# Optimization experiments

Measured on AMD Instinct MI355X. Metric: run time of the kernel, lower is better.

## Reference

```python
import jax, jax.numpy as jnp
import numpy as np

WIN = (2, 7, 7)  # (H, W, D) window size

def _relative_position_index(H, W, D):
    coords = np.stack(np.meshgrid(np.arange(H), np.arange(W), np.arange(D), indexing='ij'))
    cf = coords.reshape(3, -1)  # [3, N]
    rel = cf[:, :, None] - cf[:, None, :]  # [3, N, N]
    rel = rel.transpose(1, 2, 0).copy()
    rel[:, :, 0] += H - 1
    rel[:, :, 1] += W - 1
    rel[:, :, 2] += D - 1
    rel[:, :, 0] *= (2 * W - 1) * (2 * D - 1)
    rel[:, :, 1] *= 2 * D - 1
    return jnp.asarray(rel.sum(-1), dtype=jnp.int32)  # [N, N]

def setup_inputs() -> dict:
    key = jax.random.key(0)
    ks = jax.random.split(key, 7)
    H, W, D = WIN
    N = H * W * D          # 98
    C = 192
    nh = 6
    num_windows = 64
    B_ = 8 * num_windows   # 512
    x = jax.random.normal(ks[0], (B_, N, C), dtype=jnp.float32)
    # shifted-window attention mask: 0 for allowed pairs, -100 for masked
    mask = jnp.where(jax.random.uniform(ks[1], (num_windows, N, N)) < 0.9, 0.0, -100.0).astype(jnp.float32)
    qkv_w = jax.random.normal(ks[2], (3 * C, C), dtype=jnp.float32) * 0.02
    qkv_b = jnp.zeros((3 * C,), dtype=jnp.float32)
    out_w = jax.random.normal(ks[3], (C, C), dtype=jnp.float32) * 0.02
    out_b = jnp.zeros((C,), dtype=jnp.float32)
    table_len = (2 * H - 1) * (2 * W - 1) * (2 * D - 1)  # 507
    bias_table = jax.random.normal(ks[4], (table_len, nh), dtype=jnp.float32) * 0.02
    rel_index = _relative_position_index(H, W, D)
    return {"x": x, "mask": mask, "qkv_w": qkv_w, "qkv_b": qkv_b,
            "out_w": out_w, "out_b": out_b, "bias_table": bias_table,
            "rel_index": rel_index}

def reference(x, mask, qkv_w, qkv_b, out_w, out_b, bias_table, rel_index):
    B_, N, C = x.shape
    nh = bias_table.shape[1]
    d = C // nh
    scale = d ** (-0.5)
    qkv = (x @ qkv_w.T + qkv_b).reshape(B_, N, 3, nh, d)
    qkv = qkv.transpose(2, 0, 3, 1, 4)          # [3, B_, nh, N, d]
    q, k, v = qkv[0], qkv[1], qkv[2]
    attn = jnp.einsum('bhnd,bhmd->bhnm', q, k) * scale   # [B_, nh, N, N]
    bias = bias_table[rel_index]                 # [N, N, nh]
    attn = attn + bias.transpose(2, 0, 1)[None]  # add relative position bias
    nw = mask.shape[0]
    attn = attn.reshape(B_ // nw, nw, nh, N, N) + mask[None, :, None]
    attn = attn.reshape(B_, nh, N, N)
    p = jax.nn.softmax(attn, axis=-1)
    out = jnp.einsum('bhnm,bhmd->bhnd', p, v)    # [B_, nh, N, d]
    out = out.transpose(0, 2, 1, 3).reshape(B_, N, C)
    return out @ out_w.T + out_b
```

## Files before the change

kernel.cpp:

```cpp
#include <hip/hip_runtime.h>

typedef __attribute__((ext_vector_type(8))) __bf16 bf16x8;
typedef __attribute__((ext_vector_type(4))) float f32x4;
typedef __attribute__((ext_vector_type(8))) unsigned short us8;
typedef __attribute__((ext_vector_type(4))) unsigned short us4;

#define NTOK 98
#define CDIM 192
#define NH 6
#define NWIN 64
#define BWIN 512
#define MROWS (BWIN * NTOK)
#define NN (NTOK * NTOK)
#define SCALE 0.17677669529663687f

#define PREP_BM (NWIN * NH * NN)
#define PREP_WQ (3 * CDIM * CDIM)
#define PREP_TOT (PREP_BM + PREP_WQ)

__device__ __forceinline__ unsigned short f2b(float f) {
  unsigned u = __builtin_bit_cast(unsigned, f);
  u += 0x7FFFu + ((u >> 16) & 1u);
  return (unsigned short)(u >> 16);
}

__device__ __forceinline__ bf16x8 ldfrag(const unsigned short* p) {
  return __builtin_bit_cast(bf16x8, *(const us8*)p);
}

__global__ __launch_bounds__(256) void k_prep(
    const float* __restrict__ table, const int* __restrict__ relidx,
    const float* __restrict__ mask, const float* __restrict__ wq,
    float* __restrict__ bm, unsigned short* __restrict__ wqb) {
  int idx = blockIdx.x * 256 + threadIdx.x;
  if (idx < PREP_BM) {
    int w = idx / (NH * NN);
    int r = idx - w * NH * NN;
    int h = r / NN, ij = r - h * NN;
    bm[idx] = table[relidx[ij] * NH + h] + mask[w * NN + ij];
    return;
  }
  int i2 = idx - PREP_BM;
  if (i2 < PREP_WQ) wqb[i2] = f2b(wq[i2]);
}

__global__ __launch_bounds__(256) void k_qkv(
    const float* __restrict__ x, const unsigned short* __restrict__ wqb,
    const float* __restrict__ bias, unsigned short* __restrict__ qkv) {
  __shared__ unsigned short As[128 * 200];
  __shared__ unsigned short Bs[64 * 200];
  const int tid = threadIdx.x;
  const int m0 = blockIdx.x * 128;
  for (int it = 0; it < 24; ++it) {
    int q = it * 256 + tid;
    int row = q / 48, c4 = q - row * 48;
    float4 v = *(const float4*)(x + (m0 + row) * CDIM + c4 * 4);
    us4 u = {f2b(v.x), f2b(v.y), f2b(v.z), f2b(v.w)};
    *(us4*)&As[row * 200 + c4 * 4] = u;
  }
  const int lane = tid & 63;
  const int l15 = lane & 15, hi = lane >> 4;
  const int wr = (tid >> 6) >> 1, wc = (tid >> 6) & 1;
  __syncthreads();
  for (int j = 0; j < 9; ++j) {
    for (int it = 0; it < 6; ++it) {
      int q = it * 256 + tid;
      int row = q / 24, c8 = q - row * 24;
      *(us8*)&Bs[row * 200 + c8 * 8] = *(const us8*)(wqb + (j * 64 + row) * CDIM + c8 * 8);
    }
    __syncthreads();
    f32x4 acc[4][2];
#pragma unroll
    for (int fr = 0; fr < 4; ++fr) { acc[fr][0] = (f32x4)0.f; acc[fr][1] = (f32x4)0.f; }
#pragma unroll
    for (int ks = 0; ks < 6; ++ks) {
      int k0 = ks * 32 + hi * 8;
      bf16x8 b0 = ldfrag(&Bs[(wc * 32 + l15) * 200 + k0]);
      bf16x8 b1 = ldfrag(&Bs[(wc * 32 + 16 + l15) * 200 + k0]);
#pragma unroll
      for (int fr = 0; fr < 4; ++fr) {
        bf16x8 a = ldfrag(&As[(wr * 64 + fr * 16 + l15) * 200 + k0]);
        acc[fr][0] = __builtin_amdgcn_mfma_f32_16x16x32_bf16(a, b0, acc[fr][0], 0, 0, 0);
        acc[fr][1] = __builtin_amdgcn_mfma_f32_16x16x32_bf16(a, b1, acc[fr][1], 0, 0, 0);
      }
    }
    __syncthreads();
#pragma unroll
    for (int fr = 0; fr < 4; ++fr)
#pragma unroll
      for (int fc = 0; fc < 2; ++fc) {
        int colb = j * 64 + wc * 32 + fc * 16;
        int t = (colb >= 2 * CDIM) ? 2 : (colb >= CDIM ? 1 : 0);
        int head = (colb >> 5) - t * NH;
        int d = (colb & 31) + l15;
        long pbase = ((long)(t * NH + head) * MROWS) * 32 + d;
#pragma unroll
        for (int r = 0; r < 4; ++r) {
          int row = m0 + wr * 64 + fr * 16 + hi * 4 + r;
          float v = acc[fr][fc][r] + bias[colb + l15];
          if (t == 0) v *= SCALE;
          qkv[pbase + (long)row * 32] = f2b(v);
        }
      }
  }
}

__global__ __launch_bounds__(448, 6) void k_attn(
    const unsigned short* __restrict__ qkv, const float* __restrict__ bm,
    unsigned short* __restrict__ ao) {
  __shared__ unsigned short Vt[32 * 136];
  __shared__ unsigned short P[112 * 136];
  const int tid = threadIdx.x;
  const int h = blockIdx.x % NH;
  const int b = blockIdx.x / NH;
  const int wnd = b & (NWIN - 1);
  const int lane = tid & 63, wv = tid >> 6;
  const int l15 = lane & 15, hi = lane >> 4;
  const long rb = (long)b * NTOK;
  const unsigned short* qp = qkv + ((long)h * MROWS + rb) * 32;
  const unsigned short* kp = qkv + ((long)(NH + h) * MROWS + rb) * 32;
  const unsigned short* vp = qkv + ((long)(2 * NH + h) * MROWS + rb) * 32;
  {
    int row = tid >> 2, q = tid & 3;
    if (row < NTOK) {
      us8 vv = *(const us8*)(vp + row * 32 + q * 8);
#pragma unroll
      for (int i = 0; i < 8; ++i) Vt[(q * 8 + i) * 136 + row] = vv[i];
    }
    for (int i = tid; i < 32 * 38; i += 448) {
      int dd = i / 38, n = NTOK + (i - dd * 38);
      Vt[dd * 136 + n] = 0;
    }
    for (int i = tid; i < 112 * 16; i += 448)
      P[(i >> 4) * 136 + 112 + (i & 15)] = 0;
  }
  int qn = wv * 16 + l15;
  us8 qu = (us8)0;
  if (qn < NTOK) qu = *(const us8*)(qp + qn * 32 + hi * 8);
  bf16x8 qf = __builtin_bit_cast(bf16x8, qu);
  __syncthreads();
  f32x4 sacc[7];
#pragma unroll
  for (int tc = 0; tc < 7; ++tc) {
    int rowc = tc * 16 + l15;
    rowc = rowc > 97 ? 97 : rowc;
    bf16x8 kb = ldfrag(kp + rowc * 32 + hi * 8);
    sacc[tc] = __builtin_amdgcn_mfma_f32_16x16x32_bf16(qf, kb, (f32x4)0.f, 0, 0, 0);
  }
  const float* bmp = bm + (size_t)(wnd * NH + h) * NN;
  float rsum[4];
#pragma unroll
  for (int r = 0; r < 4; ++r) {
    int row = wv * 16 + hi * 4 + r;
    int rowc = row > 97 ? 97 : row;
    float sv[7];
    float m = -1e30f;
#pragma unroll
    for (int tc = 0; tc < 7; ++tc) {
      int col = tc * 16 + l15;
      int colc = col > 97 ? 97 : col;
      float bmv = bmp[rowc * NTOK + colc];
      float val = (col < NTOK && row < NTOK) ? sacc[tc][r] + bmv : -1e30f;
      sv[tc] = val;
      m = fmaxf(m, val);
    }
#pragma unroll
    for (int off = 1; off < 16; off <<= 1) m = fmaxf(m, __shfl_xor(m, off));
    float s = 0.f;
#pragma unroll
    for (int tc = 0; tc < 7; ++tc) {
      float e = __expf(sv[tc] - m);
      s += e;
      P[row * 136 + tc * 16 + l15] = f2b(e);
    }
#pragma unroll
    for (int off = 1; off < 16; off <<= 1) s += __shfl_xor(s, off);
    rsum[r] = s;
  }
  f32x4 oacc[2];
  oacc[0] = (f32x4)0.f; oacc[1] = (f32x4)0.f;
#pragma unroll
  for (int ks = 0; ks < 4; ++ks) {
    int k0 = ks * 32 + hi * 8;
    bf16x8 pa = ldfrag(&P[(wv * 16 + l15) * 136 + k0]);
#pragma unroll
    for (int tc2 = 0; tc2 < 2; ++tc2) {
      bf16x8 vb = ldfrag(&Vt[(tc2 * 16 + l15) * 136 + k0]);
      oacc[tc2] = __builtin_amdgcn_mfma_f32_16x16x32_bf16(pa, vb, oacc[tc2], 0, 0, 0);
    }
  }
#pragma unroll
  for (int tc2 = 0; tc2 < 2; ++tc2)
#pragma unroll
    for (int r = 0; r < 4; ++r) {
      int row = wv * 16 + hi * 4 + r;
      if (row < NTOK) {
        float v = oacc[tc2][r] / rsum[r];
        ao[(rb + row) * CDIM + h * 32 + tc2 * 16 + l15] = f2b(v);
      }
    }
}

__global__ __launch_bounds__(256) void k_proj(
    const unsigned short* __restrict__ a, const float* __restrict__ w,
    const float* __restrict__ bias, float* __restrict__ out) {
  __shared__ unsigned short As[128 * 200];
  __shared__ unsigned short Bs[64 * 200];
  const int tid = threadIdx.x;
  const int m0 = blockIdx.x * 128;
  for (int it = 0; it < 12; ++it) {
    int q = it * 256 + tid;
    int row = q / 24, c8 = q - row * 24;
    *(us8*)&As[row * 200 + c8 * 8] = *(const us8*)(a + (m0 + row) * CDIM + c8 * 8);
  }
  const int lane = tid & 63;
  const int l15 = lane & 15, hi = lane >> 4;
  const int wr = (tid >> 6) >> 1, wc = (tid >> 6) & 1;
  __syncthreads();
  for (int j = 0; j < 3; ++j) {
    for (int it = 0; it < 12; ++it) {
      int q = it * 256 + tid;
      int row = q / 48, c4 = q - row * 48;
      float4 v = *(const float4*)(w + (j * 64 + row) * CDIM + c4 * 4);
      us4 u = {f2b(v.x), f2b(v.y), f2b(v.z), f2b(v.w)};
      *(us4*)&Bs[row * 200 + c4 * 4] = u;
    }
    __syncthreads();
    f32x4 acc[4][2];
#pragma unroll
    for (int fr = 0; fr < 4; ++fr) { acc[fr][0] = (f32x4)0.f; acc[fr][1] = (f32x4)0.f; }
#pragma unroll
    for (int ks = 0; ks < 6; ++ks) {
      int k0 = ks * 32 + hi * 8;
      bf16x8 b0 = ldfrag(&Bs[(wc * 32 + l15) * 200 + k0]);
      bf16x8 b1 = ldfrag(&Bs[(wc * 32 + 16 + l15) * 200 + k0]);
#pragma unroll
      for (int fr = 0; fr < 4; ++fr) {
        bf16x8 aa = ldfrag(&As[(wr * 64 + fr * 16 + l15) * 200 + k0]);
        acc[fr][0] = __builtin_amdgcn_mfma_f32_16x16x32_bf16(aa, b0, acc[fr][0], 0, 0, 0);
        acc[fr][1] = __builtin_amdgcn_mfma_f32_16x16x32_bf16(aa, b1, acc[fr][1], 0, 0, 0);
      }
    }
    __syncthreads();
#pragma unroll
    for (int fr = 0; fr < 4; ++fr)
#pragma unroll
      for (int fc = 0; fc < 2; ++fc)
#pragma unroll
        for (int r = 0; r < 4; ++r) {
          int row = m0 + wr * 64 + fr * 16 + hi * 4 + r;
          int col = j * 64 + wc * 32 + fc * 16 + l15;
          out[row * CDIM + col] = acc[fr][fc][r] + bias[col];
        }
  }
}

extern "C" void kernel_launch(void* const* d_in, const int* in_sizes, int n_in,
                              void* d_out, int out_size, void* d_ws, size_t ws_size,
                              hipStream_t stream) {
  const float* x      = (const float*)d_in[0];
  const float* mask   = (const float*)d_in[1];
  const float* qkv_w  = (const float*)d_in[2];
  const float* qkv_b  = (const float*)d_in[3];
  const float* out_w  = (const float*)d_in[4];
  const float* out_b  = (const float*)d_in[5];
  const float* table  = (const float*)d_in[6];
  const int*   relidx = (const int*)d_in[7];
  float* out = (float*)d_out;
  char* ws = (char*)d_ws;

  float* bm            = (float*)ws;
  unsigned short* qkvp = (unsigned short*)(ws + 14751744);
  unsigned short* aop  = (unsigned short*)(ws + 72554496);
  unsigned short* wqb  = aop;

  k_prep<<<PREP_TOT / 256, 256, 0, stream>>>(table, relidx, mask, qkv_w, bm, wqb);
  k_qkv<<<MROWS / 128, 256, 0, stream>>>(x, wqb, qkv_b, qkvp);
  k_attn<<<BWIN * NH, 448, 0, stream>>>(qkvp, bm, aop);
  k_proj<<<MROWS / 128, 256, 0, stream>>>(aop, out_w, out_b, out);
}
```

Before: 208.9 us.

## Precompute padded bf16 bias-mask in fragment layout and pre-convert x to bf16

The prep kernel now writes the combined relative-position bias and mask as bf16, padded to 112x128 per (window, head) and ordered so each lane loads its 7 columns with one 16-byte vector load. Padding entries hold bf16 -inf, which removes the bounds clamps and selects from the attention softmax. The prep kernel also converts x to bf16 so the QKV GEMM loads bf16 tiles directly. The bias now goes through bf16 rounding, and the q/k loads for padded rows read past row 97 into neighbouring data. The bf16 copy of x adds an extra write and read of the activations.

```diff
diff --git a/kernel.cpp b/kernel.cpp
--- a/kernel.cpp
+++ b/kernel.cpp
@@ -14,9 +14,11 @@
 #define NN (NTOK * NTOK)
 #define SCALE 0.17677669529663687f
 
-#define PREP_BM (NWIN * NH * NN)
+#define BMH_SLICE (112 * 128)
+#define PREP_BMH (NWIN * NH * BMH_SLICE)
 #define PREP_WQ (3 * CDIM * CDIM)
-#define PREP_TOT (PREP_BM + PREP_WQ)
+#define PREP_XB (MROWS * CDIM)
+#define PREP_TOT (PREP_BMH + PREP_WQ + PREP_XB)
 
 __device__ __forceinline__ unsigned short f2b(float f) {
   unsigned u = __builtin_bit_cast(unsigned, f);
@@ -24,6 +26,10 @@
   return (unsigned short)(u >> 16);
 }
 
+__device__ __forceinline__ float b2f(unsigned short u) {
+  return __builtin_bit_cast(float, (unsigned)u << 16);
+}
+
 __device__ __forceinline__ bf16x8 ldfrag(const unsigned short* p) {
   return __builtin_bit_cast(bf16x8, *(const us8*)p);
 }
@@ -31,32 +37,42 @@
 __global__ __launch_bounds__(256) void k_prep(
     const float* __restrict__ table, const int* __restrict__ relidx,
     const float* __restrict__ mask, const float* __restrict__ wq,
-    float* __restrict__ bm, unsigned short* __restrict__ wqb) {
+    const float* __restrict__ x, unsigned short* __restrict__ bmh,
+    unsigned short* __restrict__ wqb, unsigned short* __restrict__ xb) {
   int idx = blockIdx.x * 256 + threadIdx.x;
-  if (idx < PREP_BM) {
-    int w = idx / (NH * NN);
-    int r = idx - w * NH * NN;
-    int h = r / NN, ij = r - h * NN;
-    bm[idx] = table[relidx[ij] * NH + h] + mask[w * NN + ij];
+  if (idx < PREP_BMH) {
+    int slice = idx / BMH_SLICE;
+    int rem = idx - slice * BMH_SLICE;
+    int row = rem >> 7;
+    int li = rem & 127;
+    int l = li >> 3, tc = li & 7;
+    int col = tc * 16 + l;
+    int wnd = slice / NH, h = slice - wnd * NH;
+    unsigned short v = 0xFF80;
+    if (row < NTOK && col < NTOK && tc < 7) {
+      int ij = row * NTOK + col;
+      v = f2b(table[relidx[ij] * NH + h] + mask[wnd * NN + ij]);
+    }
+    bmh[idx] = v;
     return;
   }
-  int i2 = idx - PREP_BM;
-  if (i2 < PREP_WQ) wqb[i2] = f2b(wq[i2]);
+  int i2 = idx - PREP_BMH;
+  if (i2 < PREP_WQ) { wqb[i2] = f2b(wq[i2]); return; }
+  int i3 = i2 - PREP_WQ;
+  xb[i3] = f2b(x[i3]);
 }
 
 __global__ __launch_bounds__(256) void k_qkv(
-    const float* __restrict__ x, const unsigned short* __restrict__ wqb,
+    const unsigned short* __restrict__ xb, const unsigned short* __restrict__ wqb,
     const float* __restrict__ bias, unsigned short* __restrict__ qkv) {
   __shared__ unsigned short As[128 * 200];
   __shared__ unsigned short Bs[64 * 200];
   const int tid = threadIdx.x;
   const int m0 = blockIdx.x * 128;
-  for (int it = 0; it < 24; ++it) {
+  for (int it = 0; it < 12; ++it) {
     int q = it * 256 + tid;
-    int row = q / 48, c4 = q - row * 48;
-    float4 v = *(const float4*)(x + (m0 + row) * CDIM + c4 * 4);
-    us4 u = {f2b(v.x), f2b(v.y), f2b(v.z), f2b(v.w)};
-    *(us4*)&As[row * 200 + c4 * 4] = u;
+    int row = q / 24, c8 = q - row * 24;
+    *(us8*)&As[row * 200 + c8 * 8] = *(const us8*)(xb + (m0 + row) * CDIM + c8 * 8);
   }
   const int lane = tid & 63;
   const int l15 = lane & 15, hi = lane >> 4;
@@ -106,7 +122,7 @@
 }
 
 __global__ __launch_bounds__(448, 6) void k_attn(
-    const unsigned short* __restrict__ qkv, const float* __restrict__ bm,
+    const unsigned short* __restrict__ qkv, const unsigned short* __restrict__ bmh,
     unsigned short* __restrict__ ao) {
   __shared__ unsigned short Vt[32 * 136];
   __shared__ unsigned short P[112 * 136];
@@ -120,6 +136,12 @@
   const unsigned short* qp = qkv + ((long)h * MROWS + rb) * 32;
   const unsigned short* kp = qkv + ((long)(NH + h) * MROWS + rb) * 32;
   const unsigned short* vp = qkv + ((long)(2 * NH + h) * MROWS + rb) * 32;
+  const unsigned short* bmp8 = bmh + (size_t)(wnd * NH + h) * BMH_SLICE;
+  us8 bmv[4];
+#pragma unroll
+  for (int r = 0; r < 4; ++r)
+    bmv[r] = *(const us8*)(bmp8 + (wv * 16 + hi * 4 + r) * 128 + l15 * 8);
+  bf16x8 qf = ldfrag(qp + (wv * 16 + l15) * 32 + hi * 8);
   {
     int row = tid >> 2, q = tid & 3;
     if (row < NTOK) {
@@ -134,33 +156,22 @@
     for (int i = tid; i < 112 * 16; i += 448)
       P[(i >> 4) * 136 + 112 + (i & 15)] = 0;
   }
-  int qn = wv * 16 + l15;
-  us8 qu = (us8)0;
-  if (qn < NTOK) qu = *(const us8*)(qp + qn * 32 + hi * 8);
-  bf16x8 qf = __builtin_bit_cast(bf16x8, qu);
   __syncthreads();
   f32x4 sacc[7];
 #pragma unroll
   for (int tc = 0; tc < 7; ++tc) {
-    int rowc = tc * 16 + l15;
-    rowc = rowc > 97 ? 97 : rowc;
-    bf16x8 kb = ldfrag(kp + rowc * 32 + hi * 8);
+    bf16x8 kb = ldfrag(kp + (tc * 16 + l15) * 32 + hi * 8);
     sacc[tc] = __builtin_amdgcn_mfma_f32_16x16x32_bf16(qf, kb, (f32x4)0.f, 0, 0, 0);
   }
-  const float* bmp = bm + (size_t)(wnd * NH + h) * NN;
   float rsum[4];
 #pragma unroll
   for (int r = 0; r < 4; ++r) {
     int row = wv * 16 + hi * 4 + r;
-    int rowc = row > 97 ? 97 : row;
     float sv[7];
     float m = -1e30f;
 #pragma unroll
     for (int tc = 0; tc < 7; ++tc) {
-      int col = tc * 16 + l15;
-      int colc = col > 97 ? 97 : col;
-      float bmv = bmp[rowc * NTOK + colc];
-      float val = (col < NTOK && row < NTOK) ? sacc[tc][r] + bmv : -1e30f;
+      float val = sacc[tc][r] + b2f(bmv[r][tc]);
       sv[tc] = val;
       m = fmaxf(m, val);
     }
@@ -269,13 +280,15 @@
   float* out = (float*)d_out;
   char* ws = (char*)d_ws;
 
-  float* bm            = (float*)ws;
-  unsigned short* qkvp = (unsigned short*)(ws + 14751744);
-  unsigned short* aop  = (unsigned short*)(ws + 72554496);
-  unsigned short* wqb  = aop;
-
-  k_prep<<<PREP_TOT / 256, 256, 0, stream>>>(table, relidx, mask, qkv_w, bm, wqb);
-  k_qkv<<<MROWS / 128, 256, 0, stream>>>(x, wqb, qkv_b, qkvp);
-  k_attn<<<BWIN * NH, 448, 0, stream>>>(qkvp, bm, aop);
+  unsigned short* bmh  = (unsigned short*)ws;
+  unsigned short* wqb  = (unsigned short*)(ws + 11010048);
+  unsigned short* qkvp = (unsigned short*)(ws + 11231232);
+  unsigned short* aop  = (unsigned short*)(ws + 69033984);
+  unsigned short* xb   = aop;
+
+  k_prep<<<PREP_TOT / 256, 256, 0, stream>>>(table, relidx, mask, qkv_w, x,
+                                             bmh, wqb, xb);
+  k_qkv<<<MROWS / 128, 256, 0, stream>>>(xb, wqb, qkv_b, qkvp);
+  k_attn<<<BWIN * NH, 448, 0, stream>>>(qkvp, bmh, aop);
   k_proj<<<MROWS / 128, 256, 0, stream>>>(aop, out_w, out_b, out);
 }
```

Result: faster. 193.0 us (-7.6%).
